# Kernel optimization log

Hardware: AMD Instinct MI355X
Metric: run time of the kernel (lower is better)

The kernel has to match this reference:

```python
import jax, jax.numpy as jnp
import numpy as np

HEAD_NUM = 16
HIDDEN = 1024
HEAD_DIM = HIDDEN // HEAD_NUM


def setup_inputs() -> dict:
    key = jax.random.key(0)
    ks = jax.random.split(key, 9)
    B, S, D = 1, 4096, HIDDEN
    scale = 1.0 / np.sqrt(D)
    inp = {
        "x": jax.random.normal(ks[0], (B, S, D), jnp.float32),
        "wq": jax.random.normal(ks[1], (D, D), jnp.float32) * scale,
        "bq": jnp.zeros((D,), jnp.float32),
        "wk": jax.random.normal(ks[2], (D, D), jnp.float32) * scale,
        "bk": jnp.zeros((D,), jnp.float32),
        "wv": jax.random.normal(ks[3], (D, D), jnp.float32) * scale,
        "bv": jnp.zeros((D,), jnp.float32),
        "wo": jax.random.normal(ks[4], (D, D), jnp.float32) * scale,
        "bo": jnp.zeros((D,), jnp.float32),
    }
    return inp


def reference(x, wq, bq, wk, bk, wv, bv, wo, bo):
    B, S, D = x.shape
    H, Hd = HEAD_NUM, HEAD_DIM
    # QKV projections (weights stored as [in, out])
    q = (x @ wq + bq).reshape(B, S, H, Hd).transpose(0, 2, 1, 3)  # [B,H,S,Hd]
    k = (x @ wk + bk).reshape(B, S, H, Hd).transpose(0, 2, 1, 3)
    v = (x @ wv + bv).reshape(B, S, H, Hd).transpose(0, 2, 1, 3)
    scores = jnp.einsum("bhqd,bhkd->bhqk", q, k) / jnp.sqrt(jnp.float32(Hd))
    attn = jax.nn.softmax(scores, axis=-1)  # dropout in eval mode = identity
    out = jnp.einsum("bhqk,bhkd->bhqd", attn, v)
    out = out.transpose(0, 2, 1, 3).reshape(B, S, D)
    return out @ wo + bo
```

## Files before the change

kernel.cpp:

```cpp
#include <hip/hip_runtime.h>

#define S_LEN  4096
#define DMODEL 1024
#define NHEAD  16
#define HDIM   64

#define QSCALE 0.18033688011112042f

typedef unsigned short u16;
typedef unsigned int   u32;
typedef __bf16 bf16x8 __attribute__((ext_vector_type(8)));
typedef float  f32x4  __attribute__((ext_vector_type(4)));

static __device__ __forceinline__ u16 f2b(float f) {
    union { __bf16 b; u16 u; } c; c.b = (__bf16)f; return c.u;
}

static __device__ __forceinline__ float fexp2(float x) {
#if __has_builtin(__builtin_amdgcn_exp2f)
    return __builtin_amdgcn_exp2f(x);
#else
    return __expf(x * 0.6931471805599453f);
#endif
}

typedef __attribute__((address_space(3))) u32 lds_u32_t;
typedef __attribute__((address_space(1))) const u32 glb_u32_t;
static __device__ __forceinline__ void gload_lds16(const u16* g, u16* l) {
    __builtin_amdgcn_global_load_lds((glb_u32_t*)g, (lds_u32_t*)l, 16, 0, 0);
}

__global__ __launch_bounds__(256)
void convert_x(const float* __restrict__ x, u16* __restrict__ xb) {
    const int i0 = (blockIdx.x * 256 + threadIdx.x) * 8;
    float4 a = *reinterpret_cast<const float4*>(x + i0);
    float4 b = *reinterpret_cast<const float4*>(x + i0 + 4);
    u16 o[8] = {f2b(a.x), f2b(a.y), f2b(a.z), f2b(a.w),
                f2b(b.x), f2b(b.y), f2b(b.z), f2b(b.w)};
    *reinterpret_cast<uint4*>(xb + i0) = *reinterpret_cast<uint4*>(o);
}

__global__ __launch_bounds__(256)
void transpose_w4(const float* __restrict__ w0, const float* __restrict__ w1,
                  const float* __restrict__ w2, const float* __restrict__ w3,
                  u16* __restrict__ wT) {
    const int z = blockIdx.z;
    const float* w = (z == 0) ? w0 : (z == 1) ? w1 : (z == 2) ? w2 : w3;
    u16* dst0 = wT + (size_t)z * DMODEL * DMODEL;
    const int k0 = blockIdx.x * 64, n0 = blockIdx.y * 64;
    const int t = threadIdx.x;
    __shared__ u16 T[64][72];
    const int kk = t >> 4, nn = (t & 15) * 4;
    #pragma unroll
    for (int i = 0; i < 4; ++i) {
        float4 v = *reinterpret_cast<const float4*>(w + (size_t)(k0 + kk + i * 16) * DMODEL + n0 + nn);
        T[nn + 0][kk + i * 16] = f2b(v.x);
        T[nn + 1][kk + i * 16] = f2b(v.y);
        T[nn + 2][kk + i * 16] = f2b(v.z);
        T[nn + 3][kk + i * 16] = f2b(v.w);
    }
    __syncthreads();
    const int n = t >> 2, kc = (t & 3) * 16;
    uint4 r0 = *reinterpret_cast<const uint4*>(&T[n][kc]);
    uint4 r1 = *reinterpret_cast<const uint4*>(&T[n][kc + 8]);
    u16* dst = dst0 + (size_t)(n0 + n) * DMODEL + k0 + kc;
    *reinterpret_cast<uint4*>(dst)     = r0;
    *reinterpret_cast<uint4*>(dst + 8) = r1;
}

template<int MODE>
__global__ __launch_bounds__(256, 2)
void gemm128(const u16* __restrict__ A, const u16* __restrict__ BT,
             const float* __restrict__ b0, const float* __restrict__ b1,
             const float* __restrict__ b2, void* __restrict__ Cout) {
    const int m0 = blockIdx.x * 128;
    const int ny = blockIdx.y;
    const int tz = (MODE == 0) ? (ny >> 3) : 0;
    const int n0 = (MODE == 0) ? ((ny & 7) * 128) : (ny * 128);
    const int tid = threadIdx.x, lane = tid & 63, w = tid >> 6;
    const int wr = w >> 1, wc = w & 1;
    const int fm = lane & 15, fq = lane >> 4;

    __shared__ u16 As[128][32];
    __shared__ u16 Bs[128][32];

    const u16* Bb = BT + (size_t)tz * DMODEL * DMODEL;

    f32x4 acc[4][4];
    #pragma unroll
    for (int i = 0; i < 4; ++i)
        #pragma unroll
        for (int t = 0; t < 4; ++t) acc[i][t] = f32x4{0.f, 0.f, 0.f, 0.f};

    const int srow = lane >> 2, scol = (lane & 3) * 8;

    for (int k0 = 0; k0 < DMODEL; k0 += 32) {
        #pragma unroll
        for (int r = 0; r < 2; ++r) {
            const int rowA = w * 32 + r * 16;
            gload_lds16(A  + (size_t)(m0 + rowA + srow) * DMODEL + k0 + scol, &As[rowA][0]);
            gload_lds16(Bb + (size_t)(n0 + rowA + srow) * DMODEL + k0 + scol, &Bs[rowA][0]);
        }
        __syncthreads();
        bf16x8 af[4], bf[4];
        #pragma unroll
        for (int i = 0; i < 4; ++i) af[i] = *reinterpret_cast<const bf16x8*>(&As[wr * 64 + i * 16 + fm][fq * 8]);
        #pragma unroll
        for (int t = 0; t < 4; ++t) bf[t] = *reinterpret_cast<const bf16x8*>(&Bs[wc * 64 + t * 16 + fm][fq * 8]);
        #pragma unroll
        for (int i = 0; i < 4; ++i)
            #pragma unroll
            for (int t = 0; t < 4; ++t)
                acc[i][t] = __builtin_amdgcn_mfma_f32_16x16x32_bf16(af[i], bf[t], acc[i][t], 0, 0, 0);
        __syncthreads();
    }

    const float* bp = (MODE == 0) ? ((tz == 0) ? b0 : (tz == 1) ? b1 : b2) : b0;
    const float scl = (MODE == 0 && tz == 0) ? QSCALE : 1.0f;
    #pragma unroll
    for (int t = 0; t < 4; ++t) {
        const int col = n0 + wc * 64 + t * 16 + fm;
        const float bias = bp[col];
        #pragma unroll
        for (int i = 0; i < 4; ++i) {
            #pragma unroll
            for (int r = 0; r < 4; ++r) {
                const int row = m0 + wr * 64 + i * 16 + fq * 4 + r;
                const float v = (acc[i][t][r] + bias) * scl;
                if (MODE == 0) {
                    const int hh = col >> 6, d = col & 63;
                    ((u16*)Cout)[(size_t)tz * S_LEN * DMODEL + ((size_t)hh * S_LEN + row) * HDIM + d] = f2b(v);
                } else {
                    ((float*)Cout)[(size_t)row * DMODEL + col] = v;
                }
            }
        }
    }
}

template<int NSPLIT>
__global__ __launch_bounds__(256, 4)
void attn_kernel(const u16* __restrict__ Q, const u16* __restrict__ K,
                 const u16* __restrict__ V, void* __restrict__ Optr,
                 float* __restrict__ Lp) {
    const int qt = blockIdx.x, h = blockIdx.y;
    const int sp = (NSPLIT == 2) ? blockIdx.z : 0;
    const int tid = threadIdx.x, lane = tid & 63, wid = tid >> 6;
    const int fm = lane & 15, fq = lane >> 4;

    __shared__ alignas(16) u16 Pt[128][68];
    __shared__ alignas(16) u16 Ks[64][68];
    __shared__ alignas(16) u16 Vt[64][68];

    const u16* Qh = Q + (size_t)h * S_LEN * HDIM;
    const u16* Kh = K + (size_t)h * S_LEN * HDIM;
    const u16* Vh = V + (size_t)h * S_LEN * HDIM;

    const int srow = tid >> 2, sch = (tid & 3) * 16;
    const int kp = tid & 31, vg = (tid >> 5) * 8;

    bf16x8 qf[2][2];
    #pragma unroll
    for (int rb = 0; rb < 2; ++rb) {
        const u16* qsrc = Qh + (size_t)(qt * 128 + wid * 32 + rb * 16 + fm) * HDIM + fq * 8;
        qf[rb][0] = *reinterpret_cast<const bf16x8*>(qsrc);
        qf[rb][1] = *reinterpret_cast<const bf16x8*>(qsrc + 32);
    }

    float rsum[2] = {0.f, 0.f};
    f32x4 oacc[2][4];
    #pragma unroll
    for (int rb = 0; rb < 2; ++rb)
        #pragma unroll
        for (int t = 0; t < 4; ++t) oacc[rb][t] = f32x4{0.f, 0.f, 0.f, 0.f};

    const int NT  = S_LEN / 64 / NSPLIT;
    const int kt0 = sp * NT;

    uint4 kr0, kr1, vr0, vr1;
    {
        const u16* ks = Kh + (size_t)(kt0 * 64 + srow) * HDIM + sch;
        kr0 = *reinterpret_cast<const uint4*>(ks);
        kr1 = *reinterpret_cast<const uint4*>(ks + 8);
        const u16* vs = Vh + (size_t)(kt0 * 64 + 2 * kp) * HDIM + vg;
        vr0 = *reinterpret_cast<const uint4*>(vs);
        vr1 = *reinterpret_cast<const uint4*>(vs + HDIM);
    }

    for (int it = 0; it < NT; ++it) {
        const int kt = kt0 + it;
        __syncthreads();
        *reinterpret_cast<uint4*>(&Ks[srow][sch])     = kr0;
        *reinterpret_cast<uint4*>(&Ks[srow][sch + 8]) = kr1;
        {
            union { uint4 q; u16 hw[8]; } a, b;
            a.q = vr0; b.q = vr1;
            #pragma unroll
            for (int j = 0; j < 8; ++j) {
                u32 pk = (u32)a.hw[j] | ((u32)b.hw[j] << 16);
                *reinterpret_cast<u32*>(&Vt[vg + j][2 * kp]) = pk;
            }
        }
        __syncthreads();

        if (it + 1 < NT) {
            const u16* ks = Kh + (size_t)((kt + 1) * 64 + srow) * HDIM + sch;
            kr0 = *reinterpret_cast<const uint4*>(ks);
            kr1 = *reinterpret_cast<const uint4*>(ks + 8);
            const u16* vs = Vh + (size_t)((kt + 1) * 64 + 2 * kp) * HDIM + vg;
            vr0 = *reinterpret_cast<const uint4*>(vs);
            vr1 = *reinterpret_cast<const uint4*>(vs + HDIM);
        }

        f32x4 sacc[2][4];
        #pragma unroll
        for (int rb = 0; rb < 2; ++rb)
            #pragma unroll
            for (int mt = 0; mt < 4; ++mt) sacc[rb][mt] = f32x4{0.f, 0.f, 0.f, 0.f};
        #pragma unroll
        for (int kk2 = 0; kk2 < 2; ++kk2) {
            #pragma unroll
            for (int mt = 0; mt < 4; ++mt) {
                bf16x8 kf = *reinterpret_cast<const bf16x8*>(&Ks[mt * 16 + fm][kk2 * 32 + fq * 8]);
                #pragma unroll
                for (int rb = 0; rb < 2; ++rb)
                    sacc[rb][mt] = __builtin_amdgcn_mfma_f32_16x16x32_bf16(kf, qf[rb][kk2], sacc[rb][mt], 0, 0, 0);
            }
        }

        #pragma unroll
        for (int rb = 0; rb < 2; ++rb) {
            #pragma unroll
            for (int mt = 0; mt < 4; ++mt) {
                u32 pk[2];
                float e0 = fexp2(sacc[rb][mt][0]);
                float e1 = fexp2(sacc[rb][mt][1]);
                float e2 = fexp2(sacc[rb][mt][2]);
                float e3 = fexp2(sacc[rb][mt][3]);
                rsum[rb] += (e0 + e1) + (e2 + e3);
                pk[0] = (u32)f2b(e0) | ((u32)f2b(e1) << 16);
                pk[1] = (u32)f2b(e2) | ((u32)f2b(e3) << 16);
                *reinterpret_cast<uint2*>(&Pt[wid * 32 + rb * 16 + fm][mt * 16 + fq * 4]) =
                    uint2{pk[0], pk[1]};
            }
        }

        #pragma unroll
        for (int kk2 = 0; kk2 < 2; ++kk2) {
            bf16x8 af[2];
            #pragma unroll
            for (int rb = 0; rb < 2; ++rb)
                af[rb] = *reinterpret_cast<const bf16x8*>(&Pt[wid * 32 + rb * 16 + fm][kk2 * 32 + fq * 8]);
            #pragma unroll
            for (int t = 0; t < 4; ++t) {
                bf16x8 bf = *reinterpret_cast<const bf16x8*>(&Vt[t * 16 + fm][kk2 * 32 + fq * 8]);
                #pragma unroll
                for (int rb = 0; rb < 2; ++rb)
                    oacc[rb][t] = __builtin_amdgcn_mfma_f32_16x16x32_bf16(af[rb], bf, oacc[rb][t], 0, 0, 0);
            }
        }
    }

    if (NSPLIT == 2) {
        float* Op = (float*)Optr + (size_t)sp * S_LEN * DMODEL;
        #pragma unroll
        for (int rb = 0; rb < 2; ++rb) {
            float rs = rsum[rb];
            rs += __shfl_xor(rs, 16, 64);
            rs += __shfl_xor(rs, 32, 64);
            if (fq == 0)
                Lp[(size_t)sp * NHEAD * S_LEN + (size_t)h * S_LEN +
                   qt * 128 + wid * 32 + rb * 16 + fm] = rs;
            #pragma unroll
            for (int t = 0; t < 4; ++t) {
                const int d = t * 16 + fm;
                #pragma unroll
                for (int r = 0; r < 4; ++r) {
                    const int row = qt * 128 + wid * 32 + rb * 16 + fq * 4 + r;
                    Op[(size_t)row * DMODEL + h * HDIM + d] = oacc[rb][t][r];
                }
            }
        }
    } else {
        float l[2][4];
        #pragma unroll
        for (int rb = 0; rb < 2; ++rb) {
            float rs = rsum[rb];
            rs += __shfl_xor(rs, 16, 64);
            rs += __shfl_xor(rs, 32, 64);
            #pragma unroll
            for (int r = 0; r < 4; ++r) l[rb][r] = __shfl(rs, fq * 4 + r, 64);
        }
        u16* O = (u16*)Optr;
        #pragma unroll
        for (int rb = 0; rb < 2; ++rb)
            #pragma unroll
            for (int t = 0; t < 4; ++t) {
                const int d = t * 16 + fm;
                #pragma unroll
                for (int r = 0; r < 4; ++r) {
                    const int row = qt * 128 + wid * 32 + rb * 16 + fq * 4 + r;
                    O[(size_t)row * DMODEL + h * HDIM + d] = f2b(oacc[rb][t][r] / l[rb][r]);
                }
            }
    }
}

__global__ __launch_bounds__(256)
void combine_o(const float* __restrict__ Op, const float* __restrict__ Lp,
               u16* __restrict__ Ob) {
    const size_t i = ((size_t)blockIdx.x * 256 + threadIdx.x) * 4;
    const int row = (int)(i >> 10), col = (int)(i & 1023);
    const int h = col >> 6;
    float4 a = *reinterpret_cast<const float4*>(Op + i);
    float4 b = *reinterpret_cast<const float4*>(Op + (size_t)S_LEN * DMODEL + i);
    const float l = Lp[(size_t)h * S_LEN + row] +
                    Lp[(size_t)NHEAD * S_LEN + (size_t)h * S_LEN + row];
    const float inv = 1.0f / l;
    u16 o[4] = {f2b((a.x + b.x) * inv), f2b((a.y + b.y) * inv),
                f2b((a.z + b.z) * inv), f2b((a.w + b.w) * inv)};
    *reinterpret_cast<uint2*>(Ob + i) = *reinterpret_cast<uint2*>(o);
}

extern "C" void kernel_launch(void* const* d_in, const int* in_sizes, int n_in,
                              void* d_out, int out_size, void* d_ws, size_t ws_size,
                              hipStream_t stream) {
    const float* x  = (const float*)d_in[0];
    const float* wq = (const float*)d_in[1];
    const float* bq = (const float*)d_in[2];
    const float* wk = (const float*)d_in[3];
    const float* bk = (const float*)d_in[4];
    const float* wv = (const float*)d_in[5];
    const float* bv = (const float*)d_in[6];
    const float* wo = (const float*)d_in[7];
    const float* bo = (const float*)d_in[8];

    u16* ws = (u16*)d_ws;
    const size_t MW  = (size_t)DMODEL * DMODEL;
    const size_t NX  = (size_t)S_LEN * DMODEL;
    const size_t TSZ = (size_t)NHEAD * S_LEN * HDIM;

    u16* xb = ws;
    u16* WT = xb + NX;
    u16* Qb = WT + 4 * MW;
    u16* Ob = Qb + 3 * TSZ;
    float* Op = (float*)(Ob + NX);
    float* Lp = Op + (size_t)2 * NX;
    const size_t need = (size_t)((char*)(Lp + (size_t)2 * NHEAD * S_LEN) - (char*)d_ws);
    const bool split = (ws_size >= need);

    hipLaunchKernelGGL(convert_x, dim3(NX / 2048), dim3(256), 0, stream, x, xb);
    hipLaunchKernelGGL(transpose_w4, dim3(16, 16, 4), dim3(256), 0, stream, wq, wk, wv, wo, WT);

    hipLaunchKernelGGL((gemm128<0>), dim3(S_LEN / 128, 24), dim3(256), 0, stream,
                       xb, WT, bq, bk, bv, (void*)Qb);

    if (split) {
        hipLaunchKernelGGL((attn_kernel<2>), dim3(S_LEN / 128, NHEAD, 2), dim3(256), 0, stream,
                           Qb, Qb + TSZ, Qb + 2 * TSZ, (void*)Op, Lp);
        hipLaunchKernelGGL(combine_o, dim3((S_LEN * DMODEL / 4) / 256), dim3(256), 0, stream,
                           Op, Lp, Ob);
    } else {
        hipLaunchKernelGGL((attn_kernel<1>), dim3(S_LEN / 128, NHEAD, 1), dim3(256), 0, stream,
                           Qb, Qb + TSZ, Qb + 2 * TSZ, (void*)Ob, (float*)nullptr);
    }

    hipLaunchKernelGGL((gemm128<1>), dim3(S_LEN / 128, 8), dim3(256), 0, stream,
                       Ob, WT + 3 * MW, bo, bo, bo, d_out);
}
```

Baseline: 250.7 us.

## Add 4-way key split for attention and interleave exp with PV MMA

Adds a 4-way split of the key range in attention, used when the workspace is large enough, with a generic combine kernel that sums NS partial outputs and row sums. The exp/pack step is now done in two halves, each followed by its own PV MFMA pass, which halves the P tile in shared memory. The launch-bounds occupancy hint rises from 4 to 6. The aim is more parallel blocks and higher occupancy, at the cost of doubling the fp32 partial-output traffic through the combine step.

```diff
diff --git a/kernel.cpp b/kernel.cpp
--- a/kernel.cpp
+++ b/kernel.cpp
@@ -139,16 +139,16 @@
 }
 
 template<int NSPLIT>
-__global__ __launch_bounds__(256, 4)
+__global__ __launch_bounds__(256, 6)
 void attn_kernel(const u16* __restrict__ Q, const u16* __restrict__ K,
                  const u16* __restrict__ V, void* __restrict__ Optr,
                  float* __restrict__ Lp) {
     const int qt = blockIdx.x, h = blockIdx.y;
-    const int sp = (NSPLIT == 2) ? blockIdx.z : 0;
+    const int sp = (NSPLIT > 1) ? blockIdx.z : 0;
     const int tid = threadIdx.x, lane = tid & 63, wid = tid >> 6;
     const int fm = lane & 15, fq = lane >> 4;
 
-    __shared__ alignas(16) u16 Pt[128][68];
+    __shared__ alignas(16) u16 Pt[128][36];
     __shared__ alignas(16) u16 Ks[64][68];
     __shared__ alignas(16) u16 Vt[64][68];
 
@@ -229,31 +229,31 @@
         }
 
         #pragma unroll
-        for (int rb = 0; rb < 2; ++rb) {
-            #pragma unroll
-            for (int mt = 0; mt < 4; ++mt) {
-                u32 pk[2];
-                float e0 = fexp2(sacc[rb][mt][0]);
-                float e1 = fexp2(sacc[rb][mt][1]);
-                float e2 = fexp2(sacc[rb][mt][2]);
-                float e3 = fexp2(sacc[rb][mt][3]);
-                rsum[rb] += (e0 + e1) + (e2 + e3);
-                pk[0] = (u32)f2b(e0) | ((u32)f2b(e1) << 16);
-                pk[1] = (u32)f2b(e2) | ((u32)f2b(e3) << 16);
-                *reinterpret_cast<uint2*>(&Pt[wid * 32 + rb * 16 + fm][mt * 16 + fq * 4]) =
-                    uint2{pk[0], pk[1]};
-            }
-        }
-
-        #pragma unroll
-        for (int kk2 = 0; kk2 < 2; ++kk2) {
+        for (int ph = 0; ph < 2; ++ph) {
+            #pragma unroll
+            for (int rb = 0; rb < 2; ++rb) {
+                #pragma unroll
+                for (int m2 = 0; m2 < 2; ++m2) {
+                    const int mt = ph * 2 + m2;
+                    u32 pk[2];
+                    float e0 = fexp2(sacc[rb][mt][0]);
+                    float e1 = fexp2(sacc[rb][mt][1]);
+                    float e2 = fexp2(sacc[rb][mt][2]);
+                    float e3 = fexp2(sacc[rb][mt][3]);
+                    rsum[rb] += (e0 + e1) + (e2 + e3);
+                    pk[0] = (u32)f2b(e0) | ((u32)f2b(e1) << 16);
+                    pk[1] = (u32)f2b(e2) | ((u32)f2b(e3) << 16);
+                    *reinterpret_cast<uint2*>(&Pt[wid * 32 + rb * 16 + fm][m2 * 16 + fq * 4]) =
+                        uint2{pk[0], pk[1]};
+                }
+            }
             bf16x8 af[2];
             #pragma unroll
             for (int rb = 0; rb < 2; ++rb)
-                af[rb] = *reinterpret_cast<const bf16x8*>(&Pt[wid * 32 + rb * 16 + fm][kk2 * 32 + fq * 8]);
+                af[rb] = *reinterpret_cast<const bf16x8*>(&Pt[wid * 32 + rb * 16 + fm][fq * 8]);
             #pragma unroll
             for (int t = 0; t < 4; ++t) {
-                bf16x8 bf = *reinterpret_cast<const bf16x8*>(&Vt[t * 16 + fm][kk2 * 32 + fq * 8]);
+                bf16x8 bf = *reinterpret_cast<const bf16x8*>(&Vt[t * 16 + fm][ph * 32 + fq * 8]);
                 #pragma unroll
                 for (int rb = 0; rb < 2; ++rb)
                     oacc[rb][t] = __builtin_amdgcn_mfma_f32_16x16x32_bf16(af[rb], bf, oacc[rb][t], 0, 0, 0);
@@ -261,7 +261,7 @@
         }
     }
 
-    if (NSPLIT == 2) {
+    if (NSPLIT > 1) {
         float* Op = (float*)Optr + (size_t)sp * S_LEN * DMODEL;
         #pragma unroll
         for (int rb = 0; rb < 2; ++rb) {
@@ -306,19 +306,22 @@
     }
 }
 
+template<int NS>
 __global__ __launch_bounds__(256)
 void combine_o(const float* __restrict__ Op, const float* __restrict__ Lp,
                u16* __restrict__ Ob) {
     const size_t i = ((size_t)blockIdx.x * 256 + threadIdx.x) * 4;
     const int row = (int)(i >> 10), col = (int)(i & 1023);
     const int h = col >> 6;
-    float4 a = *reinterpret_cast<const float4*>(Op + i);
-    float4 b = *reinterpret_cast<const float4*>(Op + (size_t)S_LEN * DMODEL + i);
-    const float l = Lp[(size_t)h * S_LEN + row] +
-                    Lp[(size_t)NHEAD * S_LEN + (size_t)h * S_LEN + row];
+    float ax = 0.f, ay = 0.f, az = 0.f, aw = 0.f, l = 0.f;
+    #pragma unroll
+    for (int s = 0; s < NS; ++s) {
+        float4 v = *reinterpret_cast<const float4*>(Op + (size_t)s * S_LEN * DMODEL + i);
+        ax += v.x; ay += v.y; az += v.z; aw += v.w;
+        l += Lp[(size_t)s * NHEAD * S_LEN + (size_t)h * S_LEN + row];
+    }
     const float inv = 1.0f / l;
-    u16 o[4] = {f2b((a.x + b.x) * inv), f2b((a.y + b.y) * inv),
-                f2b((a.z + b.z) * inv), f2b((a.w + b.w) * inv)};
+    u16 o[4] = {f2b(ax * inv), f2b(ay * inv), f2b(az * inv), f2b(aw * inv)};
     *reinterpret_cast<uint2*>(Ob + i) = *reinterpret_cast<uint2*>(o);
 }
 
@@ -345,9 +348,10 @@
     u16* Qb = WT + 4 * MW;
     u16* Ob = Qb + 3 * TSZ;
     float* Op = (float*)(Ob + NX);
-    float* Lp = Op + (size_t)2 * NX;
-    const size_t need = (size_t)((char*)(Lp + (size_t)2 * NHEAD * S_LEN) - (char*)d_ws);
-    const bool split = (ws_size >= need);
+    float* Lp4 = Op + (size_t)4 * NX;
+    float* Lp2 = Op + (size_t)2 * NX;
+    const size_t need4 = (size_t)((char*)(Lp4 + (size_t)4 * NHEAD * S_LEN) - (char*)d_ws);
+    const size_t need2 = (size_t)((char*)(Lp2 + (size_t)2 * NHEAD * S_LEN) - (char*)d_ws);
 
     hipLaunchKernelGGL(convert_x, dim3(NX / 2048), dim3(256), 0, stream, x, xb);
     hipLaunchKernelGGL(transpose_w4, dim3(16, 16, 4), dim3(256), 0, stream, wq, wk, wv, wo, WT);
@@ -355,11 +359,16 @@
     hipLaunchKernelGGL((gemm128<0>), dim3(S_LEN / 128, 24), dim3(256), 0, stream,
                        xb, WT, bq, bk, bv, (void*)Qb);
 
-    if (split) {
+    if (ws_size >= need4) {
+        hipLaunchKernelGGL((attn_kernel<4>), dim3(S_LEN / 128, NHEAD, 4), dim3(256), 0, stream,
+                           Qb, Qb + TSZ, Qb + 2 * TSZ, (void*)Op, Lp4);
+        hipLaunchKernelGGL((combine_o<4>), dim3((S_LEN * DMODEL / 4) / 256), dim3(256), 0, stream,
+                           Op, Lp4, Ob);
+    } else if (ws_size >= need2) {
         hipLaunchKernelGGL((attn_kernel<2>), dim3(S_LEN / 128, NHEAD, 2), dim3(256), 0, stream,
-                           Qb, Qb + TSZ, Qb + 2 * TSZ, (void*)Op, Lp);
-        hipLaunchKernelGGL(combine_o, dim3((S_LEN * DMODEL / 4) / 256), dim3(256), 0, stream,
-                           Op, Lp, Ob);
+                           Qb, Qb + TSZ, Qb + 2 * TSZ, (void*)Op, Lp2);
+        hipLaunchKernelGGL((combine_o<2>), dim3((S_LEN * DMODEL / 4) / 256), dim3(256), 0, stream,
+                           Op, Lp2, Ob);
     } else {
         hipLaunchKernelGGL((attn_kernel<1>), dim3(S_LEN / 128, NHEAD, 1), dim3(256), 0, stream,
                            Qb, Qb + TSZ, Qb + 2 * TSZ, (void*)Ob, (float*)nullptr);
```

Measured after the change: 534.5 us. 113% more time.
